# Kernel optimization log

Hardware: AMD Instinct MI355X
Metric: run time of the kernel (lower is better)

Reference implementation:

```python
import jax, jax.numpy as jnp
import numpy as np

NN, NC, E = 100000, 50000, 400000
ND, CD, HID, H, L = 43, 2, 128, 4, 4
C = HID // H  # per-head channels
SLOPE = 0.2   # GATv2 leaky_relu slope
EPS = 1e-5    # LayerNorm eps


def _ln(x, g, b):
    mu = x.mean(-1, keepdims=True)
    var = ((x - mu) ** 2).mean(-1, keepdims=True)
    return (x - mu) * jax.lax.rsqrt(var + EPS) * g + b


def _gatv2(x_src, x_dst, src, dst, wl, bl, wr, br, att, bias, n_dst):
    # GATv2Conv (PyG), bipartite, add_self_loops=False, concat heads
    xl = (x_src @ wl + bl).reshape(-1, H, C)   # source-side lin_l
    xr = (x_dst @ wr + br).reshape(-1, H, C)   # target-side lin_r
    m = jax.nn.leaky_relu(xl[src] + xr[dst], SLOPE)        # [E,H,C]
    score = jnp.einsum('ehc,hc->eh', m, att)               # [E,H]
    smax = jax.ops.segment_max(score, dst, num_segments=n_dst)
    ex = jnp.exp(score - smax[dst])
    den = jax.ops.segment_sum(ex, dst, num_segments=n_dst)
    alpha = ex / den[dst]                                  # segment softmax over incoming edges
    msg = xl[src] * alpha[:, :, None]                      # [E,H,C]
    out = jax.ops.segment_sum(msg, dst, num_segments=n_dst)
    return out.reshape(n_dst, H * C) + bias


def setup_inputs() -> dict:
    key = jax.random.key(0)
    ks = jax.random.split(key, 32)
    s = 0.05
    d = {
        'x_node': jax.random.normal(ks[0], (NN, ND), jnp.float32),
        'x_class': jax.random.normal(ks[1], (NC, CD), jnp.float32),
        'member_src': jax.random.randint(ks[2], (E,), 0, NN, jnp.int32),
        'member_dst': jax.random.randint(ks[3], (E,), 0, NC, jnp.int32),
        'contains_src': jax.random.randint(ks[4], (E,), 0, NC, jnp.int32),
        'contains_dst': jax.random.randint(ks[5], (E,), 0, NN, jnp.int32),
        'npw': jax.random.normal(ks[6], (ND, HID), jnp.float32) * s,
        'npb': jnp.zeros((HID,), jnp.float32),
        'cpw': jax.random.normal(ks[7], (CD, HID), jnp.float32) * s,
        'cpb': jnp.zeros((HID,), jnp.float32),
    }
    for pfx, i in (('n2c', 8), ('c2n', 16)):
        d[pfx + '_wl'] = jax.random.normal(ks[i], (L, HID, HID), jnp.float32) * s
        d[pfx + '_bl'] = jnp.zeros((L, HID), jnp.float32)
        d[pfx + '_wr'] = jax.random.normal(ks[i + 1], (L, HID, HID), jnp.float32) * s
        d[pfx + '_br'] = jnp.zeros((L, HID), jnp.float32)
        d[pfx + '_att'] = jax.random.normal(ks[i + 2], (L, H, C), jnp.float32) * s
        d[pfx + '_bias'] = jnp.zeros((L, HID), jnp.float32)
    d['ln_cg'] = jnp.ones((L, HID), jnp.float32)
    d['ln_cb'] = jnp.zeros((L, HID), jnp.float32)
    d['ln_ng'] = jnp.ones((L, HID), jnp.float32)
    d['ln_nb'] = jnp.zeros((L, HID), jnp.float32)
    return d


def reference(x_node, x_class, member_src, member_dst, contains_src, contains_dst,
              npw, npb, cpw, cpb,
              n2c_wl, n2c_bl, n2c_wr, n2c_br, n2c_att, n2c_bias,
              c2n_wl, c2n_bl, c2n_wr, c2n_br, c2n_att, c2n_bias,
              ln_cg, ln_cb, ln_ng, ln_nb):
    xn = x_node @ npw + npb
    xc = x_class @ cpw + cpb
    for l in range(L):
        h = _gatv2(xn, xc, member_src, member_dst,
                   n2c_wl[l], n2c_bl[l], n2c_wr[l], n2c_br[l], n2c_att[l], n2c_bias[l], NC)
        xc = _ln(xc + h, ln_cg[l], ln_cb[l])
        h = _gatv2(xc, xn, contains_src, contains_dst,
                   c2n_wl[l], c2n_bl[l], c2n_wr[l], c2n_br[l], c2n_att[l], c2n_bias[l], NN)
        xn = _ln(xn + h, ln_ng[l], ln_nb[l])
    return xc.mean(axis=0, keepdims=True)  # [1, HID]
```

## Files before the change

### kernel.cpp

```cpp
#include <hip/hip_runtime.h>

#define NNODE 100000
#define NCLS  50000
#define NEDGE 400000
#define NDIM  43
#define CDIM  2
#define HID   128
#define NHEAD 4
#define CHN   32
#define NLAY  4

typedef unsigned short u16;
typedef unsigned int u32;
typedef __attribute__((ext_vector_type(8))) short bf16x8;
typedef __attribute__((ext_vector_type(4))) float f32x4;

__device__ __forceinline__ u16 f2bf(float f) {
  u32 u = __float_as_uint(f);
  return (u16)((u + 0x7FFFu + ((u >> 16) & 1u)) >> 16);
}
__device__ __forceinline__ float bf2f(u16 h) {
  return __uint_as_float(((u32)h) << 16);
}

__global__ void proj_kernel(const float* __restrict__ X, const float* __restrict__ W,
                            const float* __restrict__ B, u16* __restrict__ Yh,
                            u16* __restrict__ Yl, int nrows, int K) {
  int t = blockIdx.x * blockDim.x + threadIdx.x;
  if (t >= nrows * HID) return;
  int i = t >> 7, j = t & (HID - 1);
  float acc = B[j];
  for (int k = 0; k < K; ++k)
    acc = fmaf(X[i * K + k], W[k * HID + j], acc);
  u16 h = f2bf(acc);
  Yh[t] = h;
  Yl[t] = f2bf(acc - bf2f(h));
}

__global__ __launch_bounds__(256) void proj_node(const float* __restrict__ X,
                                                 const float* __restrict__ W,
                                                 const float* __restrict__ B,
                                                 u16* __restrict__ Yh,
                                                 u16* __restrict__ Yl) {
  __shared__ float Ws[NDIM][HID];
  __shared__ float Xs[32][NDIM];
  const int tid = threadIdx.x;
  const int row0 = blockIdx.x * 32;

  for (int i = tid; i < NDIM * (HID / 4); i += 256) {
    int k = i >> 5, j4 = (i & 31) << 2;
    *(float4*)&Ws[k][j4] = *(const float4*)&W[(size_t)k * HID + j4];
  }
  const float* Xb = X + (size_t)row0 * NDIM;
  for (int i = tid; i < 32 * NDIM; i += 256) ((float*)Xs)[i] = Xb[i];
  __syncthreads();

  const int cg = tid & 31, rg = tid >> 5;
  const int j0 = cg * 4, r0 = rg * 4;

  float acc[4][4];
#pragma unroll
  for (int rr = 0; rr < 4; ++rr)
#pragma unroll
    for (int cc = 0; cc < 4; ++cc) acc[rr][cc] = 0.f;

#pragma unroll 4
  for (int k = 0; k < NDIM; ++k) {
    const float4 w = *(const float4*)&Ws[k][j0];
    const float wv[4] = {w.x, w.y, w.z, w.w};
    const float xx[4] = {Xs[r0 + 0][k], Xs[r0 + 1][k], Xs[r0 + 2][k], Xs[r0 + 3][k]};
#pragma unroll
    for (int rr = 0; rr < 4; ++rr)
#pragma unroll
      for (int cc = 0; cc < 4; ++cc)
        acc[rr][cc] = fmaf(xx[rr], wv[cc], acc[rr][cc]);
  }

  const float4 bv = *(const float4*)&B[j0];
  const float bb[4] = {bv.x, bv.y, bv.z, bv.w};
#pragma unroll
  for (int rr = 0; rr < 4; ++rr) {
    int gr = row0 + r0 + rr;
    ushort4 ho, lo_;
    float v0 = acc[rr][0] + bb[0], v1 = acc[rr][1] + bb[1];
    float v2 = acc[rr][2] + bb[2], v3 = acc[rr][3] + bb[3];
    ho.x = f2bf(v0); lo_.x = f2bf(v0 - bf2f(ho.x));
    ho.y = f2bf(v1); lo_.y = f2bf(v1 - bf2f(ho.y));
    ho.z = f2bf(v2); lo_.z = f2bf(v2 - bf2f(ho.z));
    ho.w = f2bf(v3); lo_.w = f2bf(v3 - bf2f(ho.w));
    *(ushort4*)&Yh[(size_t)gr * HID + j0] = ho;
    *(ushort4*)&Yl[(size_t)gr * HID + j0] = lo_;
  }
}

__global__ __launch_bounds__(256) void wprep(const float* __restrict__ n2c_wl,
                                             const float* __restrict__ n2c_wr,
                                             const float* __restrict__ c2n_wl,
                                             const float* __restrict__ c2n_wr,
                                             u16* __restrict__ wp) {
  int gid = blockIdx.x * 256 + threadIdx.x;
  int lane = gid & 63;
  int t = gid >> 6;
  int ct = t & 7, ks = (t >> 3) & 3, m = t >> 5;
  const float* Wb;
  switch (m >> 2) {
    case 0: Wb = n2c_wl; break;
    case 1: Wb = n2c_wr; break;
    case 2: Wb = c2n_wl; break;
    default: Wb = c2n_wr; break;
  }
  Wb += (size_t)(m & 3) * HID * HID;
  const int kg = lane >> 4, c = ct * 16 + (lane & 15);
  u16 hi[8], lo[8];
#pragma unroll
  for (int e = 0; e < 8; ++e) {
    float v = Wb[(size_t)(ks * 32 + kg * 8 + e) * HID + c];
    hi[e] = f2bf(v);
    lo[e] = f2bf(v - bf2f(hi[e]));
  }
  size_t base = (size_t)m * 32768 + ((size_t)(ks * 8 + ct) * 64 + lane) * 8;
#pragma unroll
  for (int e = 0; e < 8; ++e) {
    wp[base + e] = hi[e];
    wp[base + 16384 + e] = lo[e];
  }
}

#define GEMM_FRAME                                                     \
  const int tid = threadIdx.x;                                         \
  const int lane = tid & 63;                                           \
  const int wv = tid >> 6;                                             \
  const int row0 = blockIdx.x * 64 + wv * 16;                          \
  const int ri = lane & 15;                                            \
  const int kg = lane >> 4;                                            \
  int r = row0 + ri;                                                   \
  r = r < nrows ? r : nrows - 1;                                       \
  const size_t xbase = (size_t)r * HID + kg * 8;                       \
  bf16x8 Ah[4], Al[4];                                                 \
  _Pragma("unroll") for (int ks = 0; ks < 4; ++ks) {                   \
    Ah[ks] = *(const bf16x8*)&Xh[xbase + ks * 32];                     \
    Al[ks] = *(const bf16x8*)&Xl[xbase + ks * 32];                     \
  }

#define GEMM_CORE                                                                         \
  f32x4 acc[8];                                                                           \
  _Pragma("unroll") for (int ct = 0; ct < 8; ++ct) acc[ct] = (f32x4){0.f, 0.f, 0.f, 0.f}; \
  _Pragma("unroll") for (int ks = 0; ks < 4; ++ks) {                                      \
    const u16* wb = wp + ((size_t)(ks * 8) * 64 + lane) * 8;                              \
    _Pragma("unroll") for (int ct = 0; ct < 8; ++ct) {                                    \
      bf16x8 Bh = *(const bf16x8*)&wb[ct * 512];                                          \
      bf16x8 Bl = *(const bf16x8*)&wb[16384 + ct * 512];                                  \
      acc[ct] = __builtin_amdgcn_mfma_f32_16x16x32_bf16(Ah[ks], Bh, acc[ct], 0, 0, 0);    \
      acc[ct] = __builtin_amdgcn_mfma_f32_16x16x32_bf16(Al[ks], Bh, acc[ct], 0, 0, 0);    \
      acc[ct] = __builtin_amdgcn_mfma_f32_16x16x32_bf16(Ah[ks], Bl, acc[ct], 0, 0, 0);    \
    }                                                                                     \
  }

__global__ __launch_bounds__(256) void gemm_mfma_h(const u16* __restrict__ Xh,
                                                   const u16* __restrict__ Xl,
                                                   const u16* __restrict__ wp,
                                                   const float* __restrict__ B,
                                                   u16* __restrict__ Y, int nrows) {
  GEMM_FRAME
  GEMM_CORE
#pragma unroll
  for (int ct = 0; ct < 8; ++ct) {
    const float bias = B[ct * 16 + ri];
#pragma unroll
    for (int i = 0; i < 4; ++i) {
      int gr = row0 + kg * 4 + i;
      if (gr < nrows) Y[(size_t)gr * HID + ct * 16 + ri] = f2bf(acc[ct][i] + bias);
    }
  }
}

__global__ void hist_kernel(const int* __restrict__ dst, int* __restrict__ cnt) {
  int e = blockIdx.x * 256 + threadIdx.x;
  if (e < NEDGE) atomicAdd(&cnt[dst[e]], 1);
}

__global__ __launch_bounds__(256) void scan_blocks(const int* __restrict__ cnt,
                                                   int* __restrict__ pre,
                                                   int* __restrict__ bsum, int n) {
  __shared__ int sdata[256];
  const int b = blockIdx.x, t = threadIdx.x;
  const int base = b * 1024 + t * 4;
  int v[4], s = 0;
#pragma unroll
  for (int q = 0; q < 4; ++q) {
    int i = base + q;
    v[q] = (i < n) ? cnt[i] : 0;
    s += v[q];
  }
  sdata[t] = s;
  __syncthreads();
  for (int off = 1; off < 256; off <<= 1) {
    int y = (t >= off) ? sdata[t - off] : 0;
    __syncthreads();
    sdata[t] += y;
    __syncthreads();
  }
  int run = sdata[t] - s;
  if (t == 255) bsum[b] = sdata[255];
#pragma unroll
  for (int q = 0; q < 4; ++q) {
    int i = base + q;
    if (i < n) pre[i] = run;
    run += v[q];
  }
}

__global__ __launch_bounds__(128) void scan_partials(int* __restrict__ bsum, int nb) {
  __shared__ int sd[128];
  int t = threadIdx.x;
  int v = (t < nb) ? bsum[t] : 0;
  sd[t] = v;
  __syncthreads();
  for (int off = 1; off < 128; off <<= 1) {
    int y = (t >= off) ? sd[t - off] : 0;
    __syncthreads();
    sd[t] += y;
    __syncthreads();
  }
  if (t < nb) bsum[t] = sd[t] - v;
}

__global__ void finalize_rowptr(const int* __restrict__ pre, const int* __restrict__ bsum,
                                int* __restrict__ rowptr, int n) {
  int i = blockIdx.x * 256 + threadIdx.x;
  if (i < n) rowptr[i] = pre[i] + bsum[i >> 10];
  if (i == 0) rowptr[n] = NEDGE;
}

__global__ void scatter_csr(const int* __restrict__ src, const int* __restrict__ dst,
                            const int* __restrict__ rowptr, int* __restrict__ cursor,
                            int* __restrict__ csr_src) {
  int e = blockIdx.x * 256 + threadIdx.x;
  if (e >= NEDGE) return;
  int d = dst[e];
  int p = atomicAdd(&cursor[d], 1);
  csr_src[rowptr[d] + p] = src[e];
}

__global__ __launch_bounds__(256) void gat_dst(u16* __restrict__ xh,
                                               u16* __restrict__ xlo,
                                               const u16* __restrict__ flh,
                                               const u16* __restrict__ frh,
                                               const int* __restrict__ rowptr,
                                               const int* __restrict__ csr_src,
                                               const float* __restrict__ att,
                                               const float* __restrict__ bias,
                                               const float* __restrict__ g,
                                               const float* __restrict__ b,
                                               int n_dst) {
  const int wave = threadIdx.x >> 6;
  const int lane = threadIdx.x & 63;
  const int j = lane * 2;

  const float2 attv = *(const float2*)&att[j];
  const float2 bias2 = *(const float2*)&bias[j];
  const float2 g2 = *(const float2*)&g[j];
  const float2 b2 = *(const float2*)&b[j];

  const int stride = gridDim.x * 4;
  for (int d = blockIdx.x * 4 + wave; d < n_dst; d += stride) {
    const u32 rr = *(const u32*)&frh[(size_t)d * HID + j];
    const float2 xrv = make_float2(bf2f((u16)rr), bf2f((u16)(rr >> 16)));
    const int e0 = rowptr[d], e1 = rowptr[d + 1];

    float2 acc = make_float2(0.f, 0.f);
    float den = 0.f;
    int idx = e0;
    for (; idx + 3 < e1; idx += 4) {
      int s0 = csr_src[idx], s1 = csr_src[idx + 1];
      int s2 = csr_src[idx + 2], s3 = csr_src[idx + 3];
      u32 w0 = *(const u32*)&flh[(size_t)s0 * HID + j];
      u32 w1 = *(const u32*)&flh[(size_t)s1 * HID + j];
      u32 w2 = *(const u32*)&flh[(size_t)s2 * HID + j];
      u32 w3 = *(const u32*)&flh[(size_t)s3 * HID + j];
      u32 ws[4] = {w0, w1, w2, w3};
#pragma unroll
      for (int q = 0; q < 4; ++q) {
        float vx = bf2f((u16)ws[q]);
        float vy = bf2f((u16)(ws[q] >> 16));
        float m0 = vx + xrv.x; m0 = m0 > 0.f ? m0 : 0.2f * m0;
        float m1 = vy + xrv.y; m1 = m1 > 0.f ? m1 : 0.2f * m1;
        float p = fmaf(attv.x, m0, attv.y * m1);
        p += __shfl_xor(p, 8); p += __shfl_xor(p, 4);
        p += __shfl_xor(p, 2); p += __shfl_xor(p, 1);
        float e_ = __expf(p);
        acc.x = fmaf(e_, vx, acc.x);
        acc.y = fmaf(e_, vy, acc.y);
        den += e_;
      }
    }
    for (; idx < e1; ++idx) {
      const int s0 = csr_src[idx];
      u32 w0 = *(const u32*)&flh[(size_t)s0 * HID + j];
      float vx = bf2f((u16)w0);
      float vy = bf2f((u16)(w0 >> 16));
      float m0 = vx + xrv.x; m0 = m0 > 0.f ? m0 : 0.2f * m0;
      float m1 = vy + xrv.y; m1 = m1 > 0.f ? m1 : 0.2f * m1;
      float p = fmaf(attv.x, m0, attv.y * m1);
      p += __shfl_xor(p, 8); p += __shfl_xor(p, 4);
      p += __shfl_xor(p, 2); p += __shfl_xor(p, 1);
      float e_ = __expf(p);
      acc.x = fmaf(e_, vx, acc.x);
      acc.y = fmaf(e_, vy, acc.y);
      den += e_;
    }

    float2 outv = make_float2(0.f, 0.f);
    if (e1 > e0) {
      float rden = 1.0f / den;
      outv.x = acc.x * rden;
      outv.y = acc.y * rden;
    }

    const u32 hh = *(const u32*)&xh[(size_t)d * HID + j];
    const u32 ll = *(const u32*)&xlo[(size_t)d * HID + j];
    float vx = bf2f((u16)hh) + bf2f((u16)ll) + outv.x + bias2.x;
    float vy = bf2f((u16)(hh >> 16)) + bf2f((u16)(ll >> 16)) + outv.y + bias2.y;

    float s1 = vx + vy;
    float s2 = vx * vx + vy * vy;
#pragma unroll
    for (int off = 32; off > 0; off >>= 1) {
      s1 += __shfl_xor(s1, off);
      s2 += __shfl_xor(s2, off);
    }
    const float mu = s1 * (1.0f / HID);
    const float var = s2 * (1.0f / HID) - mu * mu;
    const float inv = rsqrtf(var + 1e-5f);
    float ox = (vx - mu) * inv * g2.x + b2.x;
    float oy = (vy - mu) * inv * g2.y + b2.y;

    u16 h0 = f2bf(ox); u16 l0 = f2bf(ox - bf2f(h0));
    u16 h1 = f2bf(oy); u16 l1 = f2bf(oy - bf2f(h1));
    *(u32*)&xh[(size_t)d * HID + j] = (u32)h0 | ((u32)h1 << 16);
    *(u32*)&xlo[(size_t)d * HID + j] = (u32)l0 | ((u32)l1 << 16);
  }
}

__global__ void colsum(const u16* __restrict__ xh, const u16* __restrict__ xlo,
                       float* __restrict__ acc) {
  int j = threadIdx.x;
  int per = (NCLS + gridDim.x - 1) / gridDim.x;
  int r0 = blockIdx.x * per;
  int r1 = min(r0 + per, NCLS);
  float s = 0.f;
  for (int r = r0; r < r1; ++r)
    s += bf2f(xh[(size_t)r * HID + j]) + bf2f(xlo[(size_t)r * HID + j]);
  atomicAdd(&acc[j], s);
}

__global__ void final_out(const float* __restrict__ acc, float* __restrict__ out) {
  int j = threadIdx.x;
  out[j] = acc[j] * (1.0f / NCLS);
}

extern "C" void kernel_launch(void* const* d_in, const int* in_sizes, int n_in,
                              void* d_out, int out_size, void* d_ws, size_t ws_size,
                              hipStream_t stream) {
  (void)in_sizes; (void)n_in; (void)out_size; (void)ws_size;
  const float* x_node     = (const float*)d_in[0];
  const float* x_class    = (const float*)d_in[1];
  const int* member_src   = (const int*)d_in[2];
  const int* member_dst   = (const int*)d_in[3];
  const int* contains_src = (const int*)d_in[4];
  const int* contains_dst = (const int*)d_in[5];
  const float* npw = (const float*)d_in[6];
  const float* npb = (const float*)d_in[7];
  const float* cpw = (const float*)d_in[8];
  const float* cpb = (const float*)d_in[9];
  const float* n2c_wl   = (const float*)d_in[10];
  const float* n2c_bl   = (const float*)d_in[11];
  const float* n2c_wr   = (const float*)d_in[12];
  const float* n2c_br   = (const float*)d_in[13];
  const float* n2c_att  = (const float*)d_in[14];
  const float* n2c_bias = (const float*)d_in[15];
  const float* c2n_wl   = (const float*)d_in[16];
  const float* c2n_bl   = (const float*)d_in[17];
  const float* c2n_wr   = (const float*)d_in[18];
  const float* c2n_br   = (const float*)d_in[19];
  const float* c2n_att  = (const float*)d_in[20];
  const float* c2n_bias = (const float*)d_in[21];
  const float* ln_cg = (const float*)d_in[22];
  const float* ln_cb = (const float*)d_in[23];
  const float* ln_ng = (const float*)d_in[24];
  const float* ln_nb = (const float*)d_in[25];

  u16* xnh = (u16*)d_ws;
  u16* xnl = xnh + (size_t)NNODE * HID;
  u16* xch = xnl + (size_t)NNODE * HID;
  u16* xcl = xch + (size_t)NCLS * HID;
  u16* flb = xcl + (size_t)NCLS * HID;
  u16* frn = flb + (size_t)NNODE * HID;
  u16* frc = frn + (size_t)NNODE * HID;
  float* accb = (float*)(frc + (size_t)NCLS * HID);
  int* rowptr_c = (int*)(accb + 128);
  int* csr_c    = rowptr_c + (NCLS + 1);
  int* rowptr_n = csr_c + NEDGE;
  int* csr_n    = rowptr_n + (NNODE + 1);
  int* cnt      = csr_n + NEDGE;
  int* cursor   = cnt + NNODE;
  int* pre      = cursor + NNODE;
  int* bsum     = pre + NNODE;
  u16* wp = (u16*)cnt;

  const int EB = (NEDGE + 255) / 256;
  const int GAT_BLOCKS = 2048;
  const int GB_N = (NNODE + 63) / 64;
  const int GB_C = (NCLS + 63) / 64;

  proj_node<<<NNODE / 32, 256, 0, stream>>>(x_node, npw, npb, xnh, xnl);
  proj_kernel<<<(NCLS * HID + 255) / 256, 256, 0, stream>>>(x_class, cpw, cpb, xch, xcl, NCLS, CDIM);

  hipMemsetAsync(cnt, 0, NCLS * sizeof(int), stream);
  hipMemsetAsync(cursor, 0, NCLS * sizeof(int), stream);
  hist_kernel<<<EB, 256, 0, stream>>>(member_dst, cnt);
  scan_blocks<<<(NCLS + 1023) / 1024, 256, 0, stream>>>(cnt, pre, bsum, NCLS);
  scan_partials<<<1, 128, 0, stream>>>(bsum, (NCLS + 1023) / 1024);
  finalize_rowptr<<<(NCLS + 255) / 256, 256, 0, stream>>>(pre, bsum, rowptr_c, NCLS);
  scatter_csr<<<EB, 256, 0, stream>>>(member_src, member_dst, rowptr_c, cursor, csr_c);

  hipMemsetAsync(cnt, 0, NNODE * sizeof(int), stream);
  hipMemsetAsync(cursor, 0, NNODE * sizeof(int), stream);
  hist_kernel<<<EB, 256, 0, stream>>>(contains_dst, cnt);
  scan_blocks<<<(NNODE + 1023) / 1024, 256, 0, stream>>>(cnt, pre, bsum, NNODE);
  scan_partials<<<1, 128, 0, stream>>>(bsum, (NNODE + 1023) / 1024);
  finalize_rowptr<<<(NNODE + 255) / 256, 256, 0, stream>>>(pre, bsum, rowptr_n, NNODE);
  scatter_csr<<<EB, 256, 0, stream>>>(contains_src, contains_dst, rowptr_n, cursor, csr_n);

  wprep<<<128, 256, 0, stream>>>(n2c_wl, n2c_wr, c2n_wl, c2n_wr, wp);

  gemm_mfma_h<<<GB_C, 256, 0, stream>>>(xch, xcl, wp + (size_t)4 * 32768,
                                        n2c_br, frc, NCLS);

  for (int l = 0; l < NLAY; ++l) {
    gemm_mfma_h<<<GB_N, 256, 0, stream>>>(xnh, xnl, wp + (size_t)(0 + l) * 32768,
                                          n2c_bl + l * HID, flb, NNODE);
    gemm_mfma_h<<<GB_N, 256, 0, stream>>>(xnh, xnl, wp + (size_t)(12 + l) * 32768,
                                          c2n_br + l * HID, frn, NNODE);
    gat_dst<<<GAT_BLOCKS, 256, 0, stream>>>(xch, xcl, flb, frc, rowptr_c, csr_c,
                                            n2c_att + l * HID, n2c_bias + l * HID,
                                            ln_cg + l * HID, ln_cb + l * HID, NCLS);
    gemm_mfma_h<<<GB_C, 256, 0, stream>>>(xch, xcl, wp + (size_t)(8 + l) * 32768,
                                          c2n_bl + l * HID, flb, NCLS);
    if (l < NLAY - 1) {
      gemm_mfma_h<<<GB_C, 256, 0, stream>>>(xch, xcl, wp + (size_t)(4 + l + 1) * 32768,
                                            n2c_br + (l + 1) * HID, frc, NCLS);
    }
    gat_dst<<<GAT_BLOCKS, 256, 0, stream>>>(xnh, xnl, flb, frn, rowptr_n, csr_n,
                                            c2n_att + l * HID, c2n_bias + l * HID,
                                            ln_ng + l * HID, ln_nb + l * HID, NNODE);
  }

  hipMemsetAsync(accb, 0, HID * sizeof(float), stream);
  colsum<<<256, HID, 0, stream>>>(xch, xcl, accb);
  final_out<<<1, HID, 0, stream>>>(accb, (float*)d_out);
}
```

Before: 1.088 ms.

## Process two destination nodes per wave with half-wave 4-channel lanes in gat_dst

Restructures the GAT destination kernel so each 64-lane wave handles two destination nodes, one per 32-lane half, with each lane covering 4 channels through 8-byte loads. The edge loop runs to the larger of the two degrees and masks the surplus iterations, and the reductions use fewer shuffle steps. The aim is to raise bytes per load and memory-level parallelism for the gather-bound aggregation. In exchange, degree imbalance between the paired nodes wastes lanes, and the loop relies on n_dst being even.

```diff
diff --git a/kernel.cpp b/kernel.cpp
--- a/kernel.cpp
+++ b/kernel.cpp
@@ -255,90 +255,100 @@
                                                int n_dst) {
   const int wave = threadIdx.x >> 6;
   const int lane = threadIdx.x & 63;
-  const int j = lane * 2;
-
-  const float2 attv = *(const float2*)&att[j];
-  const float2 bias2 = *(const float2*)&bias[j];
-  const float2 g2 = *(const float2*)&g[j];
-  const float2 b2 = *(const float2*)&b[j];
-
+  const int half = lane >> 5;
+  const int sub = lane & 31;
+  const int j0 = sub * 4;
+
+  const float4 attv = *(const float4*)&att[j0];
+  const float4 bias4 = *(const float4*)&bias[j0];
+  const float4 g4 = *(const float4*)&g[j0];
+  const float4 b4 = *(const float4*)&b[j0];
+
+  const int npairs = n_dst >> 1;
   const int stride = gridDim.x * 4;
-  for (int d = blockIdx.x * 4 + wave; d < n_dst; d += stride) {
-    const u32 rr = *(const u32*)&frh[(size_t)d * HID + j];
-    const float2 xrv = make_float2(bf2f((u16)rr), bf2f((u16)(rr >> 16)));
+  for (int t = blockIdx.x * 4 + wave; t < npairs; t += stride) {
+    const int d = 2 * t + half;
+    const ushort4 rr = *(const ushort4*)&frh[(size_t)d * HID + j0];
+    const float xr0 = bf2f(rr.x), xr1 = bf2f(rr.y), xr2 = bf2f(rr.z), xr3 = bf2f(rr.w);
     const int e0 = rowptr[d], e1 = rowptr[d + 1];
-
-    float2 acc = make_float2(0.f, 0.f);
-    float den = 0.f;
-    int idx = e0;
-    for (; idx + 3 < e1; idx += 4) {
-      int s0 = csr_src[idx], s1 = csr_src[idx + 1];
-      int s2 = csr_src[idx + 2], s3 = csr_src[idx + 3];
-      u32 w0 = *(const u32*)&flh[(size_t)s0 * HID + j];
-      u32 w1 = *(const u32*)&flh[(size_t)s1 * HID + j];
-      u32 w2 = *(const u32*)&flh[(size_t)s2 * HID + j];
-      u32 w3 = *(const u32*)&flh[(size_t)s3 * HID + j];
-      u32 ws[4] = {w0, w1, w2, w3};
-#pragma unroll
-      for (int q = 0; q < 4; ++q) {
-        float vx = bf2f((u16)ws[q]);
-        float vy = bf2f((u16)(ws[q] >> 16));
-        float m0 = vx + xrv.x; m0 = m0 > 0.f ? m0 : 0.2f * m0;
-        float m1 = vy + xrv.y; m1 = m1 > 0.f ? m1 : 0.2f * m1;
-        float p = fmaf(attv.x, m0, attv.y * m1);
-        p += __shfl_xor(p, 8); p += __shfl_xor(p, 4);
-        p += __shfl_xor(p, 2); p += __shfl_xor(p, 1);
-        float e_ = __expf(p);
-        acc.x = fmaf(e_, vx, acc.x);
-        acc.y = fmaf(e_, vy, acc.y);
-        den += e_;
-      }
-    }
-    for (; idx < e1; ++idx) {
-      const int s0 = csr_src[idx];
-      u32 w0 = *(const u32*)&flh[(size_t)s0 * HID + j];
-      float vx = bf2f((u16)w0);
-      float vy = bf2f((u16)(w0 >> 16));
-      float m0 = vx + xrv.x; m0 = m0 > 0.f ? m0 : 0.2f * m0;
-      float m1 = vy + xrv.y; m1 = m1 > 0.f ? m1 : 0.2f * m1;
-      float p = fmaf(attv.x, m0, attv.y * m1);
-      p += __shfl_xor(p, 8); p += __shfl_xor(p, 4);
-      p += __shfl_xor(p, 2); p += __shfl_xor(p, 1);
-      float e_ = __expf(p);
-      acc.x = fmaf(e_, vx, acc.x);
-      acc.y = fmaf(e_, vy, acc.y);
-      den += e_;
-    }
-
-    float2 outv = make_float2(0.f, 0.f);
-    if (e1 > e0) {
-      float rden = 1.0f / den;
-      outv.x = acc.x * rden;
-      outv.y = acc.y * rden;
-    }
-
-    const u32 hh = *(const u32*)&xh[(size_t)d * HID + j];
-    const u32 ll = *(const u32*)&xlo[(size_t)d * HID + j];
-    float vx = bf2f((u16)hh) + bf2f((u16)ll) + outv.x + bias2.x;
-    float vy = bf2f((u16)(hh >> 16)) + bf2f((u16)(ll >> 16)) + outv.y + bias2.y;
-
-    float s1 = vx + vy;
-    float s2 = vx * vx + vy * vy;
-#pragma unroll
-    for (int off = 32; off > 0; off >>= 1) {
+    const int deg = e1 - e0;
+    const int dego = __shfl_xor(deg, 32);
+    const int kmax = deg > dego ? deg : dego;
+
+    float a0 = 0.f, a1 = 0.f, a2 = 0.f, a3 = 0.f, den = 0.f;
+
+#define GAT_EDGE(wv, ok)                                              \
+    {                                                                 \
+      float c0 = bf2f(wv.x), c1 = bf2f(wv.y);                         \
+      float c2 = bf2f(wv.z), c3 = bf2f(wv.w);                         \
+      float m0 = c0 + xr0; m0 = m0 > 0.f ? m0 : 0.2f * m0;            \
+      float m1 = c1 + xr1; m1 = m1 > 0.f ? m1 : 0.2f * m1;            \
+      float m2 = c2 + xr2; m2 = m2 > 0.f ? m2 : 0.2f * m2;            \
+      float m3 = c3 + xr3; m3 = m3 > 0.f ? m3 : 0.2f * m3;            \
+      float p = fmaf(attv.x, m0, fmaf(attv.y, m1,                      \
+                fmaf(attv.z, m2, attv.w * m3)));                      \
+      p += __shfl_xor(p, 1);                                          \
+      p += __shfl_xor(p, 2);                                          \
+      p += __shfl_xor(p, 4);                                          \
+      float e_ = (ok) ? __expf(p) : 0.f;                              \
+      a0 = fmaf(e_, c0, a0); a1 = fmaf(e_, c1, a1);                   \
+      a2 = fmaf(e_, c2, a2); a3 = fmaf(e_, c3, a3);                   \
+      den += e_;                                                      \
+    }
+
+    int k = 0;
+    for (; k + 1 < kmax; k += 2) {
+      int idx0 = e0 + k, idx1 = e0 + k + 1;
+      bool ok0 = idx0 < e1, ok1 = idx1 < e1;
+      int i0 = min(idx0, NEDGE - 1), i1 = min(idx1, NEDGE - 1);
+      int s0 = csr_src[i0], s1 = csr_src[i1];
+      ushort4 w0 = *(const ushort4*)&flh[(size_t)s0 * HID + j0];
+      ushort4 w1 = *(const ushort4*)&flh[(size_t)s1 * HID + j0];
+      GAT_EDGE(w0, ok0)
+      GAT_EDGE(w1, ok1)
+    }
+    if (k < kmax) {
+      int idx0 = e0 + k;
+      bool ok0 = idx0 < e1;
+      int i0 = min(idx0, NEDGE - 1);
+      int s0 = csr_src[i0];
+      ushort4 w0 = *(const ushort4*)&flh[(size_t)s0 * HID + j0];
+      GAT_EDGE(w0, ok0)
+    }
+#undef GAT_EDGE
+
+    float rden = (e1 > e0) ? 1.0f / den : 0.f;
+    float o0 = a0 * rden, o1 = a1 * rden, o2 = a2 * rden, o3 = a3 * rden;
+
+    const ushort4 hh = *(const ushort4*)&xh[(size_t)d * HID + j0];
+    const ushort4 ll = *(const ushort4*)&xlo[(size_t)d * HID + j0];
+    float v0 = bf2f(hh.x) + bf2f(ll.x) + o0 + bias4.x;
+    float v1 = bf2f(hh.y) + bf2f(ll.y) + o1 + bias4.y;
+    float v2 = bf2f(hh.z) + bf2f(ll.z) + o2 + bias4.z;
+    float v3 = bf2f(hh.w) + bf2f(ll.w) + o3 + bias4.w;
+
+    float s1 = v0 + v1 + v2 + v3;
+    float s2 = v0 * v0 + v1 * v1 + v2 * v2 + v3 * v3;
+#pragma unroll
+    for (int off = 16; off > 0; off >>= 1) {
       s1 += __shfl_xor(s1, off);
       s2 += __shfl_xor(s2, off);
     }
     const float mu = s1 * (1.0f / HID);
     const float var = s2 * (1.0f / HID) - mu * mu;
     const float inv = rsqrtf(var + 1e-5f);
-    float ox = (vx - mu) * inv * g2.x + b2.x;
-    float oy = (vy - mu) * inv * g2.y + b2.y;
-
-    u16 h0 = f2bf(ox); u16 l0 = f2bf(ox - bf2f(h0));
-    u16 h1 = f2bf(oy); u16 l1 = f2bf(oy - bf2f(h1));
-    *(u32*)&xh[(size_t)d * HID + j] = (u32)h0 | ((u32)h1 << 16);
-    *(u32*)&xlo[(size_t)d * HID + j] = (u32)l0 | ((u32)l1 << 16);
+    float o0n = (v0 - mu) * inv * g4.x + b4.x;
+    float o1n = (v1 - mu) * inv * g4.y + b4.y;
+    float o2n = (v2 - mu) * inv * g4.z + b4.z;
+    float o3n = (v3 - mu) * inv * g4.w + b4.w;
+
+    ushort4 ho, lo_;
+    ho.x = f2bf(o0n); lo_.x = f2bf(o0n - bf2f(ho.x));
+    ho.y = f2bf(o1n); lo_.y = f2bf(o1n - bf2f(ho.y));
+    ho.z = f2bf(o2n); lo_.z = f2bf(o2n - bf2f(ho.z));
+    ho.w = f2bf(o3n); lo_.w = f2bf(o3n - bf2f(ho.w));
+    *(ushort4*)&xh[(size_t)d * HID + j0] = ho;
+    *(ushort4*)&xlo[(size_t)d * HID + j0] = lo_;
   }
 }
 
```

After: 1.108 ms. No clear change (+1.9%).
